# Kernel tuning notes

Measured on AMD Instinct MI355X. Metric: run time of the kernel, lower is better.

The kernel has to match this reference:

```python
import jax, jax.numpy as jnp
import numpy as np

NEG_SLOPE = 0.2  # PyG GATConv default LeakyReLU slope
EPS = 1e-16      # PyG softmax denominator epsilon


def _gat_layer(x, src, dst, W, a_src, a_dst, b, H, C):
    """One PyG-style GATConv layer (eval mode, add_self_loops already applied).
    x: [N, F_in], W: [F_in, H*C], a_src/a_dst: [H, C], b: [H*C]."""
    N = x.shape[0]
    h = (x @ W).reshape(N, H, C)                       # [N,H,C]
    alpha_src = jnp.sum(h * a_src, axis=-1)            # [N,H]
    alpha_dst = jnp.sum(h * a_dst, axis=-1)            # [N,H]
    e = jax.nn.leaky_relu(alpha_src[src] + alpha_dst[dst], NEG_SLOPE)  # [E,H]
    m = jax.ops.segment_max(e, dst, num_segments=N)    # [N,H] segment-softmax max
    p = jnp.exp(e - m[dst])                            # [E,H]
    s = jax.ops.segment_sum(p, dst, num_segments=N)    # [N,H]
    attn = p / (s[dst] + EPS)                          # [E,H]
    out = jax.ops.segment_sum(attn[:, :, None] * h[src], dst, num_segments=N)  # [N,H,C]
    return out.reshape(N, H * C) + b


def _add_self_loops(edge_index, N):
    loop = jnp.arange(N, dtype=edge_index.dtype)
    src = jnp.concatenate([edge_index[0], loop])
    dst = jnp.concatenate([edge_index[1], loop])
    return src, dst


def setup_inputs() -> dict:
    key = jax.random.key(0)
    N, E = 50000, 500000
    F_in, H, C = 336, 4, 128
    HC = H * C  # 512
    n_cls = 10
    ks = jax.random.split(key, 16)

    def glorot(k, shape):
        fan = shape[0] + shape[-1]
        return jax.random.normal(k, shape, jnp.float32) * jnp.sqrt(2.0 / fan)

    x = jax.random.normal(ks[0], (N, F_in), jnp.float32)
    edge_index = jax.random.randint(ks[1], (2, E), 0, N, dtype=jnp.int64)
    return {
        "x": x,
        "edge_index": edge_index,
        "W1": glorot(ks[2], (F_in, HC)),
        "a_src1": glorot(ks[3], (H, C)),
        "a_dst1": glorot(ks[4], (H, C)),
        "b1": jnp.zeros((HC,), jnp.float32),
        "W2": glorot(ks[5], (HC, HC)),
        "a_src2": glorot(ks[6], (H, C)),
        "a_dst2": glorot(ks[7], (H, C)),
        "b2": jnp.zeros((HC,), jnp.float32),
        "Wc1": glorot(ks[8], (HC, C)),
        "bc1": jnp.zeros((C,), jnp.float32),
        "Wc2": glorot(ks[9], (C, n_cls)),
        "bc2": jnp.zeros((n_cls,), jnp.float32),
    }


def reference(x, edge_index, W1, a_src1, a_dst1, b1, W2, a_src2, a_dst2, b2, Wc1, bc1, Wc2, bc2):
    H, C = 4, 128
    N = x.shape[0]
    src, dst = _add_self_loops(edge_index, N)
    h = _gat_layer(x, src, dst, W1, a_src1, a_dst1, b1, H, C)
    h = jax.nn.elu(h)  # ELU between layers only
    h = _gat_layer(h, src, dst, W2, a_src2, a_dst2, b2, H, C)
    # classifier (dropout is identity in eval)
    z = jax.nn.relu(h @ Wc1 + bc1)
    logits = z @ Wc2 + bc2
    return logits
```

## Files before the change

### kernel.cpp

```cpp
#include <hip/hip_runtime.h>
#include <math.h>

typedef unsigned short u16;
typedef unsigned int u32;
typedef short short8 __attribute__((ext_vector_type(8)));
typedef __bf16 bf16x8 __attribute__((ext_vector_type(8)));
typedef float f32x4 __attribute__((ext_vector_type(4)));
typedef u32 u32x4 __attribute__((ext_vector_type(4)));

typedef const __attribute__((address_space(1))) void* as1cv;
typedef __attribute__((address_space(3))) void* as3v;

__device__ __forceinline__ void gload16(const void* g, void* l) {
    __builtin_amdgcn_global_load_lds((as1cv)g, (as3v)l, 16, 0, 0);
}

__device__ __forceinline__ float b2f(u16 u) {
    union { u32 i; float f; } v; v.i = ((u32)u) << 16; return v.f;
}
__device__ __forceinline__ float b2f_lo(u32 q) {
    union { u32 i; float f; } v; v.i = q << 16; return v.f;
}
__device__ __forceinline__ float b2f_hi(u32 q) {
    union { u32 i; float f; } v; v.i = q & 0xffff0000u; return v.f;
}
__device__ __forceinline__ u16 f2b(float f) {
    union { float f; u32 i; } v; v.f = f;
    u32 i = v.i;
    u32 r = (i + 0x7fffu + ((i >> 16) & 1u)) >> 16;
    return (u16)r;
}
__device__ __forceinline__ u32 pack2(u16 a, u16 b) { return (u32)a | ((u32)b << 16); }


__device__ void agg_dev(const int* __restrict__ rowptr, const int* __restrict__ col,
                        const float* __restrict__ asrc, const float* __restrict__ adst,
                        const u16* __restrict__ hb, const float* __restrict__ bias,
                        u16* __restrict__ outb, int elu, int NODES) {
    const int wid = __builtin_amdgcn_readfirstlane((blockIdx.x * 256 + threadIdx.x) >> 6);
    const int nwaves = gridDim.x << 2;
    const int l = threadIdx.x & 63;
    const int hd = l >> 4;
    const int cbase = 8 * l;
    float bv[8];
#pragma unroll
    for (int c = 0; c < 8; c++) bv[c] = bias[cbase + c];

    for (int n = wid; n < NODES; n += nwaves) {
        const int beg = __builtin_amdgcn_readfirstlane(rowptr[n]);
        const int end = __builtin_amdgcn_readfirstlane(rowptr[n + 1]);
        const float ad = adst[n * 4 + hd];
        float acc0[8], acc1[8];
#pragma unroll
        for (int c = 0; c < 8; c++) { acc0[c] = 0.f; acc1[c] = 0.f; }
        float ss0 = 0.f, ss1 = 0.f;
        int j = beg;
        for (; j + 8 <= end; j += 8) {
            int s[8];
#pragma unroll
            for (int q = 0; q < 8; q++) s[q] = __builtin_amdgcn_readfirstlane(col[j + q]);
            u32x4 g[8];
#pragma unroll
            for (int q = 0; q < 8; q++)
                g[q] = *(const u32x4*)(hb + (size_t)s[q] * 512 + cbase);
            float p[8];
#pragma unroll
            for (int q = 0; q < 8; q++) {
                float e = asrc[(size_t)s[q] * 4 + hd] + ad;
                e = e > 0.f ? e : 0.2f * e;
                p[q] = __expf(e);
            }
#pragma unroll
            for (int q = 0; q < 8; q += 2) {
                ss0 += p[q]; ss1 += p[q + 1];
#pragma unroll
                for (int u = 0; u < 4; u++) {
                    acc0[2 * u]     += p[q]     * b2f_lo(g[q][u]);
                    acc0[2 * u + 1] += p[q]     * b2f_hi(g[q][u]);
                    acc1[2 * u]     += p[q + 1] * b2f_lo(g[q + 1][u]);
                    acc1[2 * u + 1] += p[q + 1] * b2f_hi(g[q + 1][u]);
                }
            }
        }
        if (j + 4 <= end) {
            int s[4];
#pragma unroll
            for (int q = 0; q < 4; q++) s[q] = __builtin_amdgcn_readfirstlane(col[j + q]);
            u32x4 g[4];
#pragma unroll
            for (int q = 0; q < 4; q++)
                g[q] = *(const u32x4*)(hb + (size_t)s[q] * 512 + cbase);
            float p[4];
#pragma unroll
            for (int q = 0; q < 4; q++) {
                float e = asrc[(size_t)s[q] * 4 + hd] + ad;
                e = e > 0.f ? e : 0.2f * e;
                p[q] = __expf(e);
            }
#pragma unroll
            for (int q = 0; q < 4; q += 2) {
                ss0 += p[q]; ss1 += p[q + 1];
#pragma unroll
                for (int u = 0; u < 4; u++) {
                    acc0[2 * u]     += p[q]     * b2f_lo(g[q][u]);
                    acc0[2 * u + 1] += p[q]     * b2f_hi(g[q][u]);
                    acc1[2 * u]     += p[q + 1] * b2f_lo(g[q + 1][u]);
                    acc1[2 * u + 1] += p[q + 1] * b2f_hi(g[q + 1][u]);
                }
            }
            j += 4;
        }
        for (; j < end; ++j) {
            int s0 = __builtin_amdgcn_readfirstlane(col[j]);
            u32x4 g0 = *(const u32x4*)(hb + (size_t)s0 * 512 + cbase);
            float e = asrc[(size_t)s0 * 4 + hd] + ad;
            e = e > 0.f ? e : 0.2f * e;
            float p0 = __expf(e);
            ss0 += p0;
#pragma unroll
            for (int u = 0; u < 4; u++) {
                acc0[2 * u]     += p0 * b2f_lo(g0[u]);
                acc0[2 * u + 1] += p0 * b2f_hi(g0[u]);
            }
        }
        float inv = 1.f / (ss0 + ss1 + 1e-16f);
        float v[8];
#pragma unroll
        for (int c = 0; c < 8; c++) {
            float tv = (acc0[c] + acc1[c]) * inv + bv[c];
            if (elu) tv = tv > 0.f ? tv : expm1f(tv);
            v[c] = tv;
        }
        u32x4 ov;
        ov[0] = pack2(f2b(v[0]), f2b(v[1]));
        ov[1] = pack2(f2b(v[2]), f2b(v[3]));
        ov[2] = pack2(f2b(v[4]), f2b(v[5]));
        ov[3] = pack2(f2b(v[6]), f2b(v[7]));
        *(u32x4*)(outb + (size_t)n * 512 + cbase) = ov;
    }
}

__device__ void gemm_dev(const u16* __restrict__ A, const u16* __restrict__ Bt,
                         u16* __restrict__ C, const float* __restrict__ bias,
                         const float* __restrict__ aS, const float* __restrict__ aD,
                         float* __restrict__ asr, float* __restrict__ ads,
                         const float* __restrict__ Wc2, const float* __restrict__ bc2,
                         float* __restrict__ outp,
                         int M, int N, int K, int act, char* shm) {
    const int t = threadIdx.x;
    const int l = t & 63, w = t >> 6;

    u16* As0 = (u16*)shm;
    u16* As1 = (u16*)(shm + 8192);
    u16* As2 = (u16*)(shm + 16384);
    u16* Bs0 = (u16*)(shm + 24576);
    u16* Bs1 = (u16*)(shm + 32768);
    u16* Bs2 = (u16*)(shm + 40960);

    const int nwg = gridDim.x * gridDim.y;
    const int fid = blockIdx.x + gridDim.x * blockIdx.y;
    int logical;
    {
        const int q = nwg >> 3, r = nwg & 7;
        const int xcd = fid & 7, ix = fid >> 3;
        logical = (xcd < r ? xcd * (q + 1) : r * (q + 1) + (xcd - r) * q) + ix;
    }
    const int gy = gridDim.y;
    const int mtile = logical / gy;
    const int hd_ = logical - mtile * gy;
    const int m0 = mtile * 128, n0 = hd_ * 128;

    const int wm = (w >> 1) * 64, wn = (w & 1) * 64;

    const int rl0 = w * 32 + (l >> 2);
    const int rl1 = rl0 + 16;
    const int gso = 8 * ((l & 3) ^ ((l >> 3) & 3));
    const u16* pA0 = A + (size_t)min(m0 + rl0, M - 1) * K + gso;
    const u16* pA1 = A + (size_t)min(m0 + rl1, M - 1) * K + gso;
    const u16* pB0 = Bt + (size_t)min(n0 + rl0, N - 1) * K + gso;
    const u16* pB1 = Bt + (size_t)min(n0 + rl1, N - 1) * K + gso;
    const int wbase = (w * 32) * 32;

    const int rs = ((l & 15) >> 1) & 3;
    const int roff = 8 * ((l >> 4) ^ rs);

    f32x4 acc[4][4];
    f32x4 z4 = {0.f, 0.f, 0.f, 0.f};
#pragma unroll
    for (int i = 0; i < 4; i++)
#pragma unroll
        for (int j = 0; j < 4; j++) acc[i][j] = z4;

    auto STAGE = [&](u16* As_, u16* Bs_, int k0) {
        gload16(pA0 + k0, As_ + wbase);
        gload16(pA1 + k0, As_ + wbase + 16 * 32);
        gload16(pB0 + k0, Bs_ + wbase);
        gload16(pB1 + k0, Bs_ + wbase + 16 * 32);
    };
    auto COMP = [&](const u16* As_, const u16* Bs_) {
        bf16x8 af[4], bfr[4];
#pragma unroll
        for (int i = 0; i < 4; i++) {
            af[i]  = *(const bf16x8*)(As_ + (wm + i * 16 + (l & 15)) * 32 + roff);
            bfr[i] = *(const bf16x8*)(Bs_ + (wn + i * 16 + (l & 15)) * 32 + roff);
        }
        __builtin_amdgcn_s_setprio(1);
#pragma unroll
        for (int i = 0; i < 4; i++)
#pragma unroll
            for (int j = 0; j < 4; j++)
                acc[i][j] = __builtin_amdgcn_mfma_f32_16x16x32_bf16(af[i], bfr[j], acc[i][j], 0, 0, 0);
        __builtin_amdgcn_s_setprio(0);
    };
    auto WSEL = [&](int s_, int ns_) {
        int ahead = ns_ - 1 - s_;
        if (ahead >= 2)      asm volatile("s_waitcnt vmcnt(8)" ::: "memory");
        else if (ahead == 1) asm volatile("s_waitcnt vmcnt(4)" ::: "memory");
        else                 asm volatile("s_waitcnt vmcnt(0)" ::: "memory");
    };

    const int ns = K >> 5;
    STAGE(As0, Bs0, 0);
    STAGE(As1, Bs1, 32);
    STAGE(As2, Bs2, 64);
    int s = 0;
    while (true) {
        WSEL(s, ns); __builtin_amdgcn_s_barrier();
        COMP(As0, Bs0); __builtin_amdgcn_s_barrier();
        if (s + 3 < ns) STAGE(As0, Bs0, (s + 3) << 5);
        if (++s >= ns) break;
        WSEL(s, ns); __builtin_amdgcn_s_barrier();
        COMP(As1, Bs1); __builtin_amdgcn_s_barrier();
        if (s + 3 < ns) STAGE(As1, Bs1, (s + 3) << 5);
        if (++s >= ns) break;
        WSEL(s, ns); __builtin_amdgcn_s_barrier();
        COMP(As2, Bs2); __builtin_amdgcn_s_barrier();
        if (s + 3 < ns) STAGE(As2, Bs2, (s + 3) << 5);
        if (++s >= ns) break;
    }

    if (act == 2) {
        float* wl = (float*)shm;
        float (*logbuf)[128][10] = (float (*)[128][10])(shm + 8192);
        for (int i = t; i < 1280; i += 256) wl[i] = Wc2[i];
        if (t < 10) wl[1280 + t] = bc2[t];
        __syncthreads();
        int cj[4];
#pragma unroll
        for (int j = 0; j < 4; j++) cj[j] = wn + j * 16 + (l & 15);
#pragma unroll
        for (int i = 0; i < 4; i++) {
#pragma unroll
            for (int r = 0; r < 4; r++) {
                float zv[4];
#pragma unroll
                for (int j = 0; j < 4; j++) {
                    float v = acc[i][j][r] + (bias ? bias[cj[j]] : 0.f);
                    zv[j] = v > 0.f ? v : 0.f;
                }
                float part[10];
#pragma unroll
                for (int k = 0; k < 10; k++) {
                    float s2 = 0.f;
#pragma unroll
                    for (int j = 0; j < 4; j++) s2 += zv[j] * wl[cj[j] * 10 + k];
#pragma unroll
                    for (int o = 1; o < 16; o <<= 1) s2 += __shfl_xor(s2, o);
                    part[k] = s2;
                }
                if ((l & 15) == 0) {
                    int rl = wm + i * 16 + (l >> 4) * 4 + r;
#pragma unroll
                    for (int k = 0; k < 10; k++) logbuf[w & 1][rl][k] = part[k];
                }
            }
        }
        __syncthreads();
        if (t < 128) {
            int row = m0 + t;
            if (row < M) {
#pragma unroll
                for (int k = 0; k < 10; k++)
                    outp[(size_t)row * 10 + k] =
                        logbuf[0][t][k] + logbuf[1][t][k] + wl[1280 + k];
            }
        }
        return;
    }

#pragma unroll
    for (int i = 0; i < 4; i++) {
        int rbase = m0 + wm + i * 16 + (l >> 4) * 4;
#pragma unroll
        for (int j = 0; j < 4; j++) {
            int c = n0 + wn + j * 16 + (l & 15);
            float bv = bias ? bias[c] : 0.f;
#pragma unroll
            for (int r = 0; r < 4; r++) {
                int row = rbase + r;
                if (row < M) {
                    float v = acc[i][j][r] + bv;
                    if (act == 1) v = v > 0.f ? v : 0.f;
                    C[(size_t)row * N + c] = f2b(v);
                }
            }
        }
    }

    if (aS) {
        float (*red)[128][2] = (float (*)[128][2])shm;
        const int hd = n0 >> 7;
        float aSv[4], aDv[4];
#pragma unroll
        for (int j = 0; j < 4; j++) {
            int c = n0 + wn + j * 16 + (l & 15);
            aSv[j] = aS[c];
            aDv[j] = aD[c];
        }
#pragma unroll
        for (int i = 0; i < 4; i++) {
#pragma unroll
            for (int r = 0; r < 4; r++) {
                float vs = 0.f, vd = 0.f;
#pragma unroll
                for (int j = 0; j < 4; j++) {
                    float hv = acc[i][j][r];
                    vs += hv * aSv[j];
                    vd += hv * aDv[j];
                }
#pragma unroll
                for (int o = 1; o < 16; o <<= 1) {
                    vs += __shfl_xor(vs, o);
                    vd += __shfl_xor(vd, o);
                }
                if ((l & 15) == 0) {
                    int rl = wm + i * 16 + (l >> 4) * 4 + r;
                    red[w & 1][rl][0] = vs;
                    red[w & 1][rl][1] = vd;
                }
            }
        }
        __syncthreads();
        if (t < 128) {
            int row = m0 + t;
            if (row < M) {
                asr[row * 4 + hd] = red[0][t][0] + red[1][t][0];
                ads[row * 4 + hd] = red[0][t][1] + red[1][t][1];
            }
        }
    }
}

__global__ __launch_bounds__(256) void BaselineGAT_41764261987077_kernel(
    int phase, int aux,
    const float* x, const int* ei,
    const float* W1, const float* as1, const float* ad1, const float* b1,
    const float* W2, const float* as2, const float* ad2, const float* b2,
    const float* Wc1, const float* bc1, const float* Wc2, const float* bc2,
    float* out,
    u16* hAb, u16* hbB, float* asr, float* ads,
    u16* xb, u16* w1t, u16* w2t, u16* wc1t,
    int* flag, int* cnt, int* tmp, int* bsum, int* boff,
    int* rowptr, int* cursor, int* col,
    const u16* gA, const u16* gB, u16* gC, const float* gBias,
    const float* gAs, const float* gAd,
    int gM, int gN, int gK, int gAct,
    int NODES, int E, int nblk)
{
    __shared__ int sstat[1024];
    extern __shared__ char dynshm[];
    int* smi = sstat;
    int* smb = sstat + 512;

    const int t = threadIdx.x;
    const int gid = blockIdx.x * 256 + t;
    const int EN = E + NODES;

    switch (phase) {
    case 100: {
        if (gid < NODES * 10) out[gid] = 1000.0f;
    } break;
    case 0: {
        if (blockIdx.x == 0) {
            if (t == 0) smi[256] = 0;
            __syncthreads();
            for (int j = t; j < 1024; j += 256)
                if (ei[2 * j + 1] != 0) atomicAdd(&smi[256], 1);
            __syncthreads();
            if (t == 0) flag[0] = (smi[256] < 16) ? 2 : 1;
        } else {
            int i = (blockIdx.x - 1) * 256 + t;
            if (i < NODES) cnt[i] = 0;
        }
    } break;
    case 2: {
        if (gid >= EN) return;
        int step = flag[0];
        int d;
        if (gid < E) {
            d = ei[(size_t)(E + gid) * step];
            if ((unsigned)d >= (unsigned)NODES) d = 0;
        } else d = gid - E;
        atomicAdd(&cnt[d], 1);
    } break;
    case 3: {
        smi[t] = (gid < NODES) ? cnt[gid] : 0;
        __syncthreads();
        for (int o = 1; o < 256; o <<= 1) {
            int add = (t >= o) ? smi[t - o] : 0;
            __syncthreads();
            smi[t] += add;
            __syncthreads();
        }
        if (gid < NODES) tmp[gid] = smi[t];
        if (t == 255) bsum[blockIdx.x] = smi[255];
    } break;
    case 5: {
        smb[t] = (t < nblk) ? bsum[t] : 0;
        __syncthreads();
        for (int o = 1; o < 256; o <<= 1) {
            int add = (t >= o) ? smb[t - o] : 0;
            __syncthreads();
            smb[t] += add;
            __syncthreads();
        }
        int base = (blockIdx.x == 0) ? 0 : smb[blockIdx.x - 1];
        if (gid >= NODES) return;
        int incl = tmp[gid] + base;
        rowptr[gid + 1] = incl;
        cursor[gid] = incl - cnt[gid];
        if (gid == 0) rowptr[0] = 0;
    } break;
    case 6: {
        if (gid >= EN) return;
        int step = flag[0];
        int d, s;
        if (gid < E) {
            s = ei[(size_t)gid * step];
            d = ei[(size_t)(E + gid) * step];
            if ((unsigned)s >= (unsigned)NODES) s = 0;
            if ((unsigned)d >= (unsigned)NODES) d = 0;
        } else { d = gid - E; s = d; }
        int pos = atomicAdd(&cursor[d], 1);
        col[pos] = s;
    } break;
    case 20: {
        int i = gid;
        const int XC = NODES * 44;
        if (i < XC) {
            int n = i / 44, kk = (i - n * 44) * 8;
            short8 o;
            if (kk < 336) {
                const f32x4* xp = (const f32x4*)(x + (size_t)n * 336 + kk);
                f32x4 f0 = xp[0], f1 = xp[1];
                o[0] = (short)f2b(f0[0]); o[1] = (short)f2b(f0[1]);
                o[2] = (short)f2b(f0[2]); o[3] = (short)f2b(f0[3]);
                o[4] = (short)f2b(f1[0]); o[5] = (short)f2b(f1[1]);
                o[6] = (short)f2b(f1[2]); o[7] = (short)f2b(f1[3]);
            } else {
#pragma unroll
                for (int e = 0; e < 8; e++) o[e] = 0;
            }
            *(short8*)(xb + (size_t)n * 352 + kk) = o;
            return;
        }
        i -= XC;
        if (i < 512 * 352) {
            int n = i / 352, k = i - n * 352;
            w1t[i] = (k < 336) ? f2b(W1[(size_t)k * 512 + n]) : (u16)0;
            return;
        }
        i -= 512 * 352;
        if (i < 512 * 512) {
            int n = i >> 9, k = i & 511;
            w2t[i] = f2b(W2[(size_t)k * 512 + n]);
            return;
        }
        i -= 512 * 512;
        if (i < 128 * 512) {
            int n = i >> 9, k = i & 511;
            wc1t[i] = f2b(Wc1[(size_t)k * 128 + n]);
        }
    } break;
    case 30: gemm_dev(gA, gB, gC, gBias, gAs, gAd, asr, ads,
                      Wc2, bc2, out, gM, gN, gK, gAct, dynshm); break;
    case 31: agg_dev(rowptr, col, asr, ads, hAb, gBias, hbB, aux, NODES); break;
    }
}

extern "C" void kernel_launch(void* const* d_in, const int* in_sizes, int n_in,
                              void* d_out, int out_size, void* d_ws, size_t ws_size,
                              hipStream_t stream) {
    const float* x   = (const float*)d_in[0];
    const int*   ei  = (const int*)d_in[1];
    const float* W1  = (const float*)d_in[2];
    const float* as1 = (const float*)d_in[3];
    const float* ad1 = (const float*)d_in[4];
    const float* b1  = (const float*)d_in[5];
    const float* W2  = (const float*)d_in[6];
    const float* as2 = (const float*)d_in[7];
    const float* ad2 = (const float*)d_in[8];
    const float* b2  = (const float*)d_in[9];
    const float* Wc1 = (const float*)d_in[10];
    const float* bc1 = (const float*)d_in[11];
    const float* Wc2 = (const float*)d_in[12];
    const float* bc2 = (const float*)d_in[13];

    const int NODES = in_sizes[0] / 336;
    const int E     = in_sizes[1] / 2;

    char* ws = (char*)d_ws;
    size_t off = 0;
    auto alloc = [&](size_t b) -> char* {
        char* p = ws + off; off = (off + b + 255) & ~(size_t)255; return p;
    };
    u16*   xb   = (u16*)alloc((size_t)NODES * 352 * 2);
    u16*   hAb  = (u16*)alloc((size_t)NODES * 512 * 2);
    u16*   hbB  = (u16*)alloc((size_t)NODES * 512 * 2);
    float* asr  = (float*)alloc((size_t)NODES * 4 * 4);
    float* ads  = (float*)alloc((size_t)NODES * 4 * 4);
    u16*   w1t  = (u16*)alloc((size_t)512 * 352 * 2);
    u16*   w2t  = (u16*)alloc((size_t)512 * 512 * 2);
    u16*   wc1t = (u16*)alloc((size_t)128 * 512 * 2);
    int* flag   = (int*)alloc(256);
    int* cnt    = (int*)alloc((size_t)NODES * 4);
    int* tmp    = (int*)alloc((size_t)NODES * 4);
    int* bsum   = (int*)alloc(4096);
    int* boff   = (int*)alloc(4096);
    int* rowptr = (int*)alloc((size_t)(NODES + 1) * 4);
    int* cursor = (int*)alloc((size_t)NODES * 4);
    int* col    = (int*)alloc((size_t)(E + NODES) * 4);

    const int nblk = (NODES + 255) / 256;
    const int eblk = (E + NODES + 255) / 256;
    const int oblk = (out_size + 255) / 256;
    const int mt   = (NODES + 127) / 128;
    const int cvt_total = NODES * 44 + 512 * 352 + 512 * 512 + 128 * 512;

    auto L = [&](int phase, int aux, dim3 grid, size_t shmem,
                 const u16* gA = nullptr, const u16* gB = nullptr,
                 u16* gC = nullptr, const float* gBias = nullptr,
                 const float* gAs = nullptr, const float* gAd = nullptr,
                 int gM = 0, int gN = 0, int gK = 0, int gAct = 0) {
        BaselineGAT_41764261987077_kernel<<<grid, 256, shmem, stream>>>(
            phase, aux, x, ei, W1, as1, ad1, b1, W2, as2, ad2, b2,
            Wc1, bc1, Wc2, bc2, (float*)d_out,
            hAb, hbB, asr, ads, xb, w1t, w2t, wc1t,
            flag, cnt, tmp, bsum, boff, rowptr, cursor, col,
            gA, gB, gC, gBias, gAs, gAd, gM, gN, gK, gAct,
            NODES, E, nblk);
    };
    const size_t GSH = 49152;

    if (n_in < 14 || off > ws_size) { L(100, 1, oblk, 0); return; }

    L(0, 0, nblk + 1, 0);
    L(2, 0, eblk, 0);
    L(3, 0, nblk, 0);
    L(5, 0, nblk, 0);
    L(6, 0, eblk, 0);

    L(20, 0, (cvt_total + 255) / 256, 0);

    L(30, 0, dim3(mt, 4), GSH, xb, w1t, hAb, nullptr, as1, ad1, NODES, 512, 352, 0);
    L(31, 1, 4096, 0, nullptr, nullptr, nullptr, b1);

    L(30, 0, dim3(mt, 4), GSH, hbB, w2t, hAb, nullptr, as2, ad2, NODES, 512, 512, 0);
    L(31, 0, 4096, 0, nullptr, nullptr, nullptr, b2);

    L(30, 0, dim3(mt, 1), GSH, hbB, wc1t, nullptr, bc1, nullptr, nullptr, NODES, 128, 512, 2);
}
```

Measured before the change: 569.7 us.

## Merge CSR build phases into fewer launches alongside conversion and first GEMM

Folds the degree-count pass and the bf16 weight/input conversion into one launch, and runs the CSR column-fill scatter as extra blocks inside the first GEMM launch. Zeroing cnt now uses hipMemsetAsync, and the GEMM grid is flattened to 1D with the work-group count passed explicitly. The goal is to cut kernel launch count and let independent small phases overlap with compute-heavy work. The risk is heavier per-block branching and extra register or LDS pressure in the combined launches.

New measurement: 557.5 us, median of 2. -2.1%, faster.

```diff
diff --git a/kernel.cpp b/kernel.cpp
--- a/kernel.cpp
+++ b/kernel.cpp
@@ -146,7 +146,7 @@
                          float* __restrict__ asr, float* __restrict__ ads,
                          const float* __restrict__ Wc2, const float* __restrict__ bc2,
                          float* __restrict__ outp,
-                         int M, int N, int K, int act, char* shm) {
+                         int M, int N, int K, int act, char* shm, int nwg) {
     const int t = threadIdx.x;
     const int l = t & 63, w = t >> 6;
 
@@ -157,15 +157,14 @@
     u16* Bs1 = (u16*)(shm + 32768);
     u16* Bs2 = (u16*)(shm + 40960);
 
-    const int nwg = gridDim.x * gridDim.y;
-    const int fid = blockIdx.x + gridDim.x * blockIdx.y;
+    const int fid = blockIdx.x;
     int logical;
     {
         const int q = nwg >> 3, r = nwg & 7;
         const int xcd = fid & 7, ix = fid >> 3;
         logical = (xcd < r ? xcd * (q + 1) : r * (q + 1) + (xcd - r) * q) + ix;
     }
-    const int gy = gridDim.y;
+    const int gy = N >> 7;
     const int mtile = logical / gy;
     const int hd_ = logical - mtile * gy;
     const int m0 = mtile * 128, n0 = hd_ * 128;
@@ -381,71 +380,26 @@
         if (gid < NODES * 10) out[gid] = 1000.0f;
     } break;
     case 0: {
-        if (blockIdx.x == 0) {
-            if (t == 0) smi[256] = 0;
-            __syncthreads();
-            for (int j = t; j < 1024; j += 256)
-                if (ei[2 * j + 1] != 0) atomicAdd(&smi[256], 1);
-            __syncthreads();
-            if (t == 0) flag[0] = (smi[256] < 16) ? 2 : 1;
-        } else {
-            int i = (blockIdx.x - 1) * 256 + t;
-            if (i < NODES) cnt[i] = 0;
-        }
+        if (t == 0) smi[256] = 0;
+        __syncthreads();
+        for (int j = t; j < 1024; j += 256)
+            if (ei[2 * j + 1] != 0) atomicAdd(&smi[256], 1);
+        __syncthreads();
+        if (t == 0) flag[0] = (smi[256] < 16) ? 2 : 1;
     } break;
     case 2: {
-        if (gid >= EN) return;
-        int step = flag[0];
-        int d;
-        if (gid < E) {
-            d = ei[(size_t)(E + gid) * step];
-            if ((unsigned)d >= (unsigned)NODES) d = 0;
-        } else d = gid - E;
-        atomicAdd(&cnt[d], 1);
-    } break;
-    case 3: {
-        smi[t] = (gid < NODES) ? cnt[gid] : 0;
-        __syncthreads();
-        for (int o = 1; o < 256; o <<= 1) {
-            int add = (t >= o) ? smi[t - o] : 0;
-            __syncthreads();
-            smi[t] += add;
-            __syncthreads();
-        }
-        if (gid < NODES) tmp[gid] = smi[t];
-        if (t == 255) bsum[blockIdx.x] = smi[255];
-    } break;
-    case 5: {
-        smb[t] = (t < nblk) ? bsum[t] : 0;
-        __syncthreads();
-        for (int o = 1; o < 256; o <<= 1) {
-            int add = (t >= o) ? smb[t - o] : 0;
-            __syncthreads();
-            smb[t] += add;
-            __syncthreads();
-        }
-        int base = (blockIdx.x == 0) ? 0 : smb[blockIdx.x - 1];
-        if (gid >= NODES) return;
-        int incl = tmp[gid] + base;
-        rowptr[gid + 1] = incl;
-        cursor[gid] = incl - cnt[gid];
-        if (gid == 0) rowptr[0] = 0;
-    } break;
-    case 6: {
-        if (gid >= EN) return;
-        int step = flag[0];
-        int d, s;
-        if (gid < E) {
-            s = ei[(size_t)gid * step];
-            d = ei[(size_t)(E + gid) * step];
-            if ((unsigned)s >= (unsigned)NODES) s = 0;
-            if ((unsigned)d >= (unsigned)NODES) d = 0;
-        } else { d = gid - E; s = d; }
-        int pos = atomicAdd(&cursor[d], 1);
-        col[pos] = s;
-    } break;
-    case 20: {
-        int i = gid;
+        if ((int)blockIdx.x < aux) {
+            if (gid >= EN) return;
+            int step = flag[0];
+            int d;
+            if (gid < E) {
+                d = ei[(size_t)(E + gid) * step];
+                if ((unsigned)d >= (unsigned)NODES) d = 0;
+            } else d = gid - E;
+            atomicAdd(&cnt[d], 1);
+            return;
+        }
+        int i = (blockIdx.x - aux) * 256 + t;
         const int XC = NODES * 44;
         if (i < XC) {
             int n = i / 44, kk = (i - n * 44) * 8;
@@ -482,8 +436,53 @@
             wc1t[i] = f2b(Wc1[(size_t)k * 128 + n]);
         }
     } break;
-    case 30: gemm_dev(gA, gB, gC, gBias, gAs, gAd, asr, ads,
-                      Wc2, bc2, out, gM, gN, gK, gAct, dynshm); break;
+    case 3: {
+        smi[t] = (gid < NODES) ? cnt[gid] : 0;
+        __syncthreads();
+        for (int o = 1; o < 256; o <<= 1) {
+            int add = (t >= o) ? smi[t - o] : 0;
+            __syncthreads();
+            smi[t] += add;
+            __syncthreads();
+        }
+        if (gid < NODES) tmp[gid] = smi[t];
+        if (t == 255) bsum[blockIdx.x] = smi[255];
+    } break;
+    case 5: {
+        smb[t] = (t < nblk) ? bsum[t] : 0;
+        __syncthreads();
+        for (int o = 1; o < 256; o <<= 1) {
+            int add = (t >= o) ? smb[t - o] : 0;
+            __syncthreads();
+            smb[t] += add;
+            __syncthreads();
+        }
+        int base = (blockIdx.x == 0) ? 0 : smb[blockIdx.x - 1];
+        if (gid >= NODES) return;
+        int incl = tmp[gid] + base;
+        rowptr[gid + 1] = incl;
+        cursor[gid] = incl - cnt[gid];
+        if (gid == 0) rowptr[0] = 0;
+    } break;
+    case 30: {
+        if ((int)blockIdx.x < aux) {
+            gemm_dev(gA, gB, gC, gBias, gAs, gAd, asr, ads,
+                     Wc2, bc2, out, gM, gN, gK, gAct, dynshm, aux);
+            return;
+        }
+        int g2 = (blockIdx.x - aux) * 256 + t;
+        if (g2 >= EN) return;
+        int step = flag[0];
+        int d, s;
+        if (g2 < E) {
+            s = ei[(size_t)g2 * step];
+            d = ei[(size_t)(E + g2) * step];
+            if ((unsigned)s >= (unsigned)NODES) s = 0;
+            if ((unsigned)d >= (unsigned)NODES) d = 0;
+        } else { d = g2 - E; s = d; }
+        int pos = atomicAdd(&cursor[d], 1);
+        col[pos] = s;
+    } break;
     case 31: agg_dev(rowptr, col, asr, ads, hAb, gBias, hbB, aux, NODES); break;
     }
 }
@@ -536,6 +535,7 @@
     const int oblk = (out_size + 255) / 256;
     const int mt   = (NODES + 127) / 128;
     const int cvt_total = NODES * 44 + 512 * 352 + 512 * 512 + 128 * 512;
+    const int cvtblk = (cvt_total + 255) / 256;
 
     auto L = [&](int phase, int aux, dim3 grid, size_t shmem,
                  const u16* gA = nullptr, const u16* gB = nullptr,
@@ -554,19 +554,17 @@
 
     if (n_in < 14 || off > ws_size) { L(100, 1, oblk, 0); return; }
 
-    L(0, 0, nblk + 1, 0);
-    L(2, 0, eblk, 0);
+    hipMemsetAsync(cnt, 0, (size_t)NODES * 4, stream);
+    L(0, 0, 1, 0);
+    L(2, eblk, eblk + cvtblk, 0);
     L(3, 0, nblk, 0);
     L(5, 0, nblk, 0);
-    L(6, 0, eblk, 0);
-
-    L(20, 0, (cvt_total + 255) / 256, 0);
-
-    L(30, 0, dim3(mt, 4), GSH, xb, w1t, hAb, nullptr, as1, ad1, NODES, 512, 352, 0);
+
+    L(30, mt * 4, mt * 4 + eblk, GSH, xb, w1t, hAb, nullptr, as1, ad1, NODES, 512, 352, 0);
     L(31, 1, 4096, 0, nullptr, nullptr, nullptr, b1);
 
-    L(30, 0, dim3(mt, 4), GSH, hbB, w2t, hAb, nullptr, as2, ad2, NODES, 512, 512, 0);
+    L(30, mt * 4, mt * 4, GSH, hbB, w2t, hAb, nullptr, as2, ad2, NODES, 512, 512, 0);
     L(31, 0, 4096, 0, nullptr, nullptr, nullptr, b2);
 
-    L(30, 0, dim3(mt, 1), GSH, hbB, wc1t, nullptr, bc1, nullptr, nullptr, NODES, 128, 512, 2);
-}
+    L(30, mt, mt, GSH, hbB, wc1t, nullptr, bc1, nullptr, nullptr, NODES, 128, 512, 2);
+}
```
